# Optimization experiments

Measured on AMD Instinct MI355X. Metric: run time of the kernel, lower is better.

The kernel has to match this reference:

```python
import jax, jax.numpy as jnp
import numpy as np


def setup_inputs() -> dict:
    key = jax.random.key(0)
    k1, k2 = jax.random.split(key)
    B, C, M, N = 8, 3, 4096, 4096
    pc_src = jax.random.normal(k1, (B, C, M), dtype=jnp.float32)
    pc_dst = jax.random.normal(k2, (B, C, N), dtype=jnp.float32)
    return {"pc_src": pc_src, "pc_dst": pc_dst}


def reference(pc_src, pc_dst):
    # pc_src: [B,3,M], pc_dst: [B,3,N]
    # Pairwise Euclidean distance via ||s||^2 + ||d||^2 - 2 s.d (avoids Bx3xMxN tensor)
    s2 = jnp.sum(pc_src * pc_src, axis=1)              # [B,M]
    d2 = jnp.sum(pc_dst * pc_dst, axis=1)              # [B,N]
    cross = jnp.einsum('bcm,bcn->bmn', pc_src, pc_dst)  # [B,M,N]
    sq = s2[:, :, None] + d2[:, None, :] - 2.0 * cross
    diff = jnp.sqrt(jnp.maximum(sq, 0.0))              # [B,M,N] L2 distances
    forward_loss = jnp.mean(jnp.min(diff, axis=2))     # src -> dst nearest
    backward_loss = jnp.mean(jnp.min(diff, axis=1))    # dst -> src nearest
    chamfer_pure = forward_loss + backward_loss
    chamfer_weighted = chamfer_pure
    return (forward_loss + backward_loss, chamfer_pure, chamfer_weighted)
```

## Files before the change

kernel.cpp:

```cpp
#include <hip/hip_runtime.h>
#include <math.h>


constexpr int B = 8;
constexpr int M = 4096;

typedef __attribute__((ext_vector_type(8)))  short bf16x8;
typedef __attribute__((ext_vector_type(16))) float f32x16;

__device__ inline unsigned short bf16_of(float x) {
    unsigned int u = __float_as_uint(x);
    u += 0x7FFFu + ((u >> 16) & 1u);
    return (unsigned short)(u >> 16);
}
__device__ inline float bf16_to_f(unsigned short h) {
    return __uint_as_float(((unsigned int)h) << 16);
}


__global__ __launch_bounds__(256, 4) void chamfer_main(
    const float* __restrict__ src,
    const float* __restrict__ dst,
    float* __restrict__ part)
{
    int bid = blockIdx.x;
    const int cs  = bid & 1;  bid >>= 1;
    const int rg  = bid & 31; bid >>= 5;
    const int b   = bid & 7;  bid >>= 3;
    const int dir = bid;

    const float* __restrict__ qry = dir ? dst : src;
    const float* __restrict__ ref = dir ? src : dst;

    const int tid  = threadIdx.x;
    const int wave = tid >> 6;
    const int l31  = tid & 31;
    const int hf   = (tid >> 5) & 1;

    __shared__ __align__(16) unsigned short bstage[2][1024][8];
    __shared__ float bsum[8];

    bf16x8 afrag;
    {
        const int mrow = rg * 128 + wave * 32 + l31;
        const float* qb = qry + (size_t)b * 3 * M;
        const float x = qb[0 * M + mrow];
        const float y = qb[1 * M + mrow];
        const float z = qb[2 * M + mrow];
        const float s2 = x * x + y * y + z * z;
        const float xhf = bf16_to_f(bf16_of(x));
        const float yhf = bf16_to_f(bf16_of(y));
        const float zhf = bf16_to_f(bf16_of(z));
        const unsigned short nxh = bf16_of(-2.0f * xhf), nxl = bf16_of(-2.0f * (x - xhf));
        const unsigned short nyh = bf16_of(-2.0f * yhf), nyl = bf16_of(-2.0f * (y - yhf));
        const unsigned short nzh = bf16_of(-2.0f * zhf), nzl = bf16_of(-2.0f * (z - zhf));
        const unsigned short s2h = bf16_of(s2);
        const unsigned short s2l = bf16_of(s2 - bf16_to_f(s2h));
        const unsigned short one = 0x3F80;
        bf16x8 alo, ahi;
        alo[0]=(short)nxh; alo[1]=(short)nxh; alo[2]=(short)nxl; alo[3]=(short)nxl;
        alo[4]=(short)nyh; alo[5]=(short)nyh; alo[6]=(short)nyl; alo[7]=(short)nyl;
        ahi[0]=(short)nzh; ahi[1]=(short)nzh; ahi[2]=(short)nzl; ahi[3]=(short)nzl;
        ahi[4]=(short)s2h; ahi[5]=(short)s2l; ahi[6]=(short)one; ahi[7]=(short)one;
        afrag = hf ? ahi : alo;
    }

    f32x16 fwdE, fwdO;
#pragma unroll
    for (int r = 0; r < 16; ++r) { fwdE[r] = 3.0e38f; fwdO[r] = 3.0e38f; }

    const f32x16 zero = {};
    const float* rb = ref + (size_t)b * 3 * M + cs * 2048;

    for (int ch = 0; ch < 2; ++ch) {
        __syncthreads();
        {
            const int c0 = tid * 4;
            const float4 vx = *reinterpret_cast<const float4*>(&rb[0 * M + ch * 1024 + c0]);
            const float4 vy = *reinterpret_cast<const float4*>(&rb[1 * M + ch * 1024 + c0]);
            const float4 vz = *reinterpret_cast<const float4*>(&rb[2 * M + ch * 1024 + c0]);
            const float xs[4] = {vx.x, vx.y, vx.z, vx.w};
            const float ys[4] = {vy.x, vy.y, vy.z, vy.w};
            const float zs[4] = {vz.x, vz.y, vz.z, vz.w};
#pragma unroll
            for (int k = 0; k < 4; ++k) {
                const float x = xs[k], y = ys[k], z = zs[k];
                const float d2 = x * x + y * y + z * z;
                const unsigned short xh = bf16_of(x), xl = bf16_of(x - bf16_to_f(xh));
                const unsigned short yh = bf16_of(y), yl = bf16_of(y - bf16_to_f(yh));
                const unsigned short zh = bf16_of(z), zl = bf16_of(z - bf16_to_f(zh));
                const unsigned short d2h = bf16_of(d2);
                const unsigned short d2l = bf16_of(d2 - bf16_to_f(d2h));
                const unsigned short one = 0x3F80;
                bf16x8 v0, v1;
                v0[0]=(short)xh; v0[1]=(short)xl; v0[2]=(short)xh; v0[3]=(short)xl;
                v0[4]=(short)yh; v0[5]=(short)yl; v0[6]=(short)yh; v0[7]=(short)yl;
                v1[0]=(short)zh; v1[1]=(short)zl; v1[2]=(short)zh; v1[3]=(short)zl;
                v1[4]=(short)one; v1[5]=(short)one; v1[6]=(short)d2h; v1[7]=(short)d2l;
                *reinterpret_cast<bf16x8*>(&bstage[0][c0 + k][0]) = v0;
                *reinterpret_cast<bf16x8*>(&bstage[1][c0 + k][0]) = v1;
            }
        }
        __syncthreads();

#pragma unroll 4
        for (int i = 0; i < 16; ++i) {
            const bf16x8 bf0 = *reinterpret_cast<const bf16x8*>(&bstage[hf][i * 64 + l31][0]);
            const bf16x8 bf1 = *reinterpret_cast<const bf16x8*>(&bstage[hf][i * 64 + 32 + l31][0]);
            const f32x16 acc0 = __builtin_amdgcn_mfma_f32_32x32x16_bf16(afrag, bf0, zero, 0, 0, 0);
            const f32x16 acc1 = __builtin_amdgcn_mfma_f32_32x32x16_bf16(afrag, bf1, zero, 0, 0, 0);
#pragma unroll
            for (int r = 0; r < 16; ++r) {
                fwdE[r] = fminf(fwdE[r], acc0[r]);
                fwdO[r] = fminf(fwdO[r], acc1[r]);
            }
        }
    }

    f32x16 fwd;
#pragma unroll
    for (int r = 0; r < 16; ++r) fwd[r] = fminf(fwdE[r], fwdO[r]);

#pragma unroll
    for (int r = 0; r < 16; ++r) {
        float vv = fwd[r];
        vv = fminf(vv, __shfl_xor(vv, 1));
        vv = fminf(vv, __shfl_xor(vv, 2));
        vv = fminf(vv, __shfl_xor(vv, 4));
        vv = fminf(vv, __shfl_xor(vv, 8));
        vv = fminf(vv, __shfl_xor(vv, 16));
        fwd[r] = vv;
    }
    if (l31 == 0) {
        float* pf = part + ((size_t)cs * 16 + dir * 8 + b) * M
                  + rg * 128 + wave * 32 + hf * 4;
#pragma unroll
        for (int r = 0; r < 16; ++r)
            pf[(r & 3) + 8 * (r >> 2)] = fwd[r];
    }
    (void)bsum;
}

__global__ __launch_bounds__(256) void chamfer_reduce(
    const float* __restrict__ part, float* __restrict__ bsums)
{
    const int idx = blockIdx.x * 256 + threadIdx.x;
    const int row = idx & (M - 1);
    const int db  = idx >> 12;

    const float* p = part + (size_t)db * M + row;
    const float v = fminf(p[0], p[(size_t)16 * M]);

    float s = sqrtf(fmaxf(v, 0.0f));
#pragma unroll
    for (int off = 32; off > 0; off >>= 1) s += __shfl_down(s, off);
    __shared__ float partial[4];
    if ((threadIdx.x & 63) == 0) partial[threadIdx.x >> 6] = s;
    __syncthreads();
    if (threadIdx.x == 0)
        bsums[blockIdx.x] = partial[0] + partial[1] + partial[2] + partial[3];
}

__global__ __launch_bounds__(256) void chamfer_final(
    const float* __restrict__ bsums, float* __restrict__ out)
{
    float s = bsums[threadIdx.x];
#pragma unroll
    for (int off = 32; off > 0; off >>= 1) s += __shfl_down(s, off);
    __shared__ float partial[4];
    if ((threadIdx.x & 63) == 0) partial[threadIdx.x >> 6] = s;
    __syncthreads();
    if (threadIdx.x == 0) {
        const float tot = (partial[0] + partial[1] + partial[2] + partial[3])
                        * (1.0f / (float)(B * M));
        out[0] = tot;
        out[1] = tot;
        out[2] = tot;
    }
}

extern "C" void kernel_launch(void* const* d_in, const int* in_sizes, int n_in,
                              void* d_out, int out_size, void* d_ws, size_t ws_size,
                              hipStream_t stream)
{
    const float* src = (const float*)d_in[0];
    const float* dst = (const float*)d_in[1];
    float* out = (float*)d_out;

    float* part  = (float*)d_ws;
    float* bsums = (float*)((char*)d_ws + (1u << 19));

    chamfer_main  <<<1024, 256, 0, stream>>>(src, dst, part);
    chamfer_reduce<<<256, 256, 0, stream>>>(part, bsums);
    chamfer_final <<<1, 256, 0, stream>>>(bsums, out);
}
```

Measured before the change: 23.01 us.

## Split reference points four ways, swizzle LDS staging, and merge min accumulators

Each block now covers a quarter of the reference points instead of half, which doubles the grid to 2048 blocks and halves the LDS staging buffer. The reduce kernel takes the min over four partials instead of two. LDS rows are XOR-swizzled to cut bank conflicts on the MFMA operand reads, and the two min accumulators are folded into one to free registers for higher occupancy. In exchange it adds more partial traffic, more per-block query setup, and a larger workspace.

```diff
diff --git a/kernel.cpp b/kernel.cpp
--- a/kernel.cpp
+++ b/kernel.cpp
@@ -18,13 +18,13 @@
 }
 
 
-__global__ __launch_bounds__(256, 4) void chamfer_main(
+__global__ __launch_bounds__(256, 6) void chamfer_main(
     const float* __restrict__ src,
     const float* __restrict__ dst,
     float* __restrict__ part)
 {
     int bid = blockIdx.x;
-    const int cs  = bid & 1;  bid >>= 1;
+    const int cs  = bid & 3;  bid >>= 2;
     const int rg  = bid & 31; bid >>= 5;
     const int b   = bid & 7;  bid >>= 3;
     const int dir = bid;
@@ -37,8 +37,10 @@
     const int l31  = tid & 31;
     const int hf   = (tid >> 5) & 1;
 
-    __shared__ __align__(16) unsigned short bstage[2][1024][8];
-    __shared__ float bsum[8];
+    __shared__ __align__(16) unsigned short bstage[2][512][8];
+
+    const int sA = l31 ^ (l31 >> 3);
+    const int sB = 32 + (l31 ^ (4 + (l31 >> 3)));
 
     bf16x8 afrag;
     {
@@ -65,25 +67,25 @@
         afrag = hf ? ahi : alo;
     }
 
-    f32x16 fwdE, fwdO;
+    f32x16 fwd;
 #pragma unroll
-    for (int r = 0; r < 16; ++r) { fwdE[r] = 3.0e38f; fwdO[r] = 3.0e38f; }
+    for (int r = 0; r < 16; ++r) fwd[r] = 3.0e38f;
 
     const f32x16 zero = {};
-    const float* rb = ref + (size_t)b * 3 * M + cs * 2048;
+    const float* rb = ref + (size_t)b * 3 * M + cs * 1024;
 
     for (int ch = 0; ch < 2; ++ch) {
         __syncthreads();
         {
-            const int c0 = tid * 4;
-            const float4 vx = *reinterpret_cast<const float4*>(&rb[0 * M + ch * 1024 + c0]);
-            const float4 vy = *reinterpret_cast<const float4*>(&rb[1 * M + ch * 1024 + c0]);
-            const float4 vz = *reinterpret_cast<const float4*>(&rb[2 * M + ch * 1024 + c0]);
-            const float xs[4] = {vx.x, vx.y, vx.z, vx.w};
-            const float ys[4] = {vy.x, vy.y, vy.z, vy.w};
-            const float zs[4] = {vz.x, vz.y, vz.z, vz.w};
+            const int c0 = tid * 2;
+            const float2 vx = *reinterpret_cast<const float2*>(&rb[0 * M + ch * 512 + c0]);
+            const float2 vy = *reinterpret_cast<const float2*>(&rb[1 * M + ch * 512 + c0]);
+            const float2 vz = *reinterpret_cast<const float2*>(&rb[2 * M + ch * 512 + c0]);
+            const float xs[2] = {vx.x, vx.y};
+            const float ys[2] = {vy.x, vy.y};
+            const float zs[2] = {vz.x, vz.y};
 #pragma unroll
-            for (int k = 0; k < 4; ++k) {
+            for (int k = 0; k < 2; ++k) {
                 const float x = xs[k], y = ys[k], z = zs[k];
                 const float d2 = x * x + y * y + z * z;
                 const unsigned short xh = bf16_of(x), xl = bf16_of(x - bf16_to_f(xh));
@@ -97,29 +99,25 @@
                 v0[4]=(short)yh; v0[5]=(short)yl; v0[6]=(short)yh; v0[7]=(short)yl;
                 v1[0]=(short)zh; v1[1]=(short)zl; v1[2]=(short)zh; v1[3]=(short)zl;
                 v1[4]=(short)one; v1[5]=(short)one; v1[6]=(short)d2h; v1[7]=(short)d2l;
-                *reinterpret_cast<bf16x8*>(&bstage[0][c0 + k][0]) = v0;
-                *reinterpret_cast<bf16x8*>(&bstage[1][c0 + k][0]) = v1;
+                const int c = c0 + k;
+                const int swz = c ^ ((c >> 3) & 7);
+                *reinterpret_cast<bf16x8*>(&bstage[0][swz][0]) = v0;
+                *reinterpret_cast<bf16x8*>(&bstage[1][swz][0]) = v1;
             }
         }
         __syncthreads();
 
-#pragma unroll 4
-        for (int i = 0; i < 16; ++i) {
-            const bf16x8 bf0 = *reinterpret_cast<const bf16x8*>(&bstage[hf][i * 64 + l31][0]);
-            const bf16x8 bf1 = *reinterpret_cast<const bf16x8*>(&bstage[hf][i * 64 + 32 + l31][0]);
+#pragma unroll
+        for (int i = 0; i < 8; ++i) {
+            const bf16x8 bf0 = *reinterpret_cast<const bf16x8*>(&bstage[hf][i * 64 + sA][0]);
+            const bf16x8 bf1 = *reinterpret_cast<const bf16x8*>(&bstage[hf][i * 64 + sB][0]);
             const f32x16 acc0 = __builtin_amdgcn_mfma_f32_32x32x16_bf16(afrag, bf0, zero, 0, 0, 0);
             const f32x16 acc1 = __builtin_amdgcn_mfma_f32_32x32x16_bf16(afrag, bf1, zero, 0, 0, 0);
 #pragma unroll
-            for (int r = 0; r < 16; ++r) {
-                fwdE[r] = fminf(fwdE[r], acc0[r]);
-                fwdO[r] = fminf(fwdO[r], acc1[r]);
-            }
+            for (int r = 0; r < 16; ++r)
+                fwd[r] = fminf(fwd[r], fminf(acc0[r], acc1[r]));
         }
     }
-
-    f32x16 fwd;
-#pragma unroll
-    for (int r = 0; r < 16; ++r) fwd[r] = fminf(fwdE[r], fwdO[r]);
 
 #pragma unroll
     for (int r = 0; r < 16; ++r) {
@@ -138,7 +136,6 @@
         for (int r = 0; r < 16; ++r)
             pf[(r & 3) + 8 * (r >> 2)] = fwd[r];
     }
-    (void)bsum;
 }
 
 __global__ __launch_bounds__(256) void chamfer_reduce(
@@ -149,7 +146,8 @@
     const int db  = idx >> 12;
 
     const float* p = part + (size_t)db * M + row;
-    const float v = fminf(p[0], p[(size_t)16 * M]);
+    const float v = fminf(fminf(p[0],                  p[(size_t)16 * M]),
+                          fminf(p[(size_t)32 * M],     p[(size_t)48 * M]));
 
     float s = sqrtf(fmaxf(v, 0.0f));
 #pragma unroll
@@ -188,9 +186,9 @@
     float* out = (float*)d_out;
 
     float* part  = (float*)d_ws;
-    float* bsums = (float*)((char*)d_ws + (1u << 19));
+    float* bsums = (float*)((char*)d_ws + (1u << 20));
 
-    chamfer_main  <<<1024, 256, 0, stream>>>(src, dst, part);
+    chamfer_main  <<<2048, 256, 0, stream>>>(src, dst, part);
     chamfer_reduce<<<256, 256, 0, stream>>>(part, bsums);
     chamfer_final <<<1, 256, 0, stream>>>(bsums, out);
 }
```

New measurement: 31.93 us. 1.39x slower.

## Swizzle LDS staging and defer cross-lane min reduction to reduce kernel

Applied to the files above, without the earlier changes.

Reference-point fragments are now written to LDS with a swizzled row index, and the MFMA B-fragment reads use the matching addressing, to avoid bank conflicts. The main kernel no longer runs the five-step shuffle min across 32 lanes. Each lane writes its partial minima to a workspace 32 times larger, and the reduce kernel now reads 32 partials per row with float4 loads and takes their min. This trades the shuffle work in the main kernel for much more global memory write and read traffic (about 16 MB of partials), and the bsums offset moves to match.

```diff
diff --git a/kernel.cpp b/kernel.cpp
--- a/kernel.cpp
+++ b/kernel.cpp
@@ -38,7 +38,8 @@
     const int hf   = (tid >> 5) & 1;
 
     __shared__ __align__(16) unsigned short bstage[2][1024][8];
-    __shared__ float bsum[8];
+
+    const int lds_base = ((l31 & 7) << 7) + (l31 >> 3);
 
     bf16x8 afrag;
     {
@@ -97,16 +98,18 @@
                 v0[4]=(short)yh; v0[5]=(short)yl; v0[6]=(short)yh; v0[7]=(short)yl;
                 v1[0]=(short)zh; v1[1]=(short)zl; v1[2]=(short)zh; v1[3]=(short)zl;
                 v1[4]=(short)one; v1[5]=(short)one; v1[6]=(short)d2h; v1[7]=(short)d2l;
-                *reinterpret_cast<bf16x8*>(&bstage[0][c0 + k][0]) = v0;
-                *reinterpret_cast<bf16x8*>(&bstage[1][c0 + k][0]) = v1;
+                const int c = c0 + k;
+                const int swz = ((c & 7) << 7) + (c >> 3);
+                *reinterpret_cast<bf16x8*>(&bstage[0][swz][0]) = v0;
+                *reinterpret_cast<bf16x8*>(&bstage[1][swz][0]) = v1;
             }
         }
         __syncthreads();
 
 #pragma unroll 4
         for (int i = 0; i < 16; ++i) {
-            const bf16x8 bf0 = *reinterpret_cast<const bf16x8*>(&bstage[hf][i * 64 + l31][0]);
-            const bf16x8 bf1 = *reinterpret_cast<const bf16x8*>(&bstage[hf][i * 64 + 32 + l31][0]);
+            const bf16x8 bf0 = *reinterpret_cast<const bf16x8*>(&bstage[hf][lds_base + i * 8][0]);
+            const bf16x8 bf1 = *reinterpret_cast<const bf16x8*>(&bstage[hf][lds_base + i * 8 + 4][0]);
             const f32x16 acc0 = __builtin_amdgcn_mfma_f32_32x32x16_bf16(afrag, bf0, zero, 0, 0, 0);
             const f32x16 acc1 = __builtin_amdgcn_mfma_f32_32x32x16_bf16(afrag, bf1, zero, 0, 0, 0);
 #pragma unroll
@@ -117,28 +120,15 @@
         }
     }
 
-    f32x16 fwd;
-#pragma unroll
-    for (int r = 0; r < 16; ++r) fwd[r] = fminf(fwdE[r], fwdO[r]);
-
-#pragma unroll
-    for (int r = 0; r < 16; ++r) {
-        float vv = fwd[r];
-        vv = fminf(vv, __shfl_xor(vv, 1));
-        vv = fminf(vv, __shfl_xor(vv, 2));
-        vv = fminf(vv, __shfl_xor(vv, 4));
-        vv = fminf(vv, __shfl_xor(vv, 8));
-        vv = fminf(vv, __shfl_xor(vv, 16));
-        fwd[r] = vv;
-    }
-    if (l31 == 0) {
-        float* pf = part + ((size_t)cs * 16 + dir * 8 + b) * M
-                  + rg * 128 + wave * 32 + hf * 4;
-#pragma unroll
-        for (int r = 0; r < 16; ++r)
-            pf[(r & 3) + 8 * (r >> 2)] = fwd[r];
-    }
-    (void)bsum;
+    {
+        float* pf = part + (((size_t)cs * 16 + (size_t)dir * 8 + b) * 4096
+                            + rg * 128 + wave * 32 + hf * 4) * 32 + l31;
+#pragma unroll
+        for (int r = 0; r < 16; ++r) {
+            const float v = fminf(fwdE[r], fwdO[r]);
+            pf[(size_t)((r & 3) + 8 * (r >> 2)) * 32] = v;
+        }
+    }
 }
 
 __global__ __launch_bounds__(256) void chamfer_reduce(
@@ -148,8 +138,22 @@
     const int row = idx & (M - 1);
     const int db  = idx >> 12;
 
-    const float* p = part + (size_t)db * M + row;
-    const float v = fminf(p[0], p[(size_t)16 * M]);
+    const float4* p0 = reinterpret_cast<const float4*>(
+        part + ((size_t)(0 * 16 + db) * 4096 + row) * 32);
+    const float4* p1 = reinterpret_cast<const float4*>(
+        part + ((size_t)(1 * 16 + db) * 4096 + row) * 32);
+
+    float m0 = 3.0e38f, m1 = 3.0e38f, m2 = 3.0e38f, m3 = 3.0e38f;
+#pragma unroll
+    for (int j = 0; j < 8; ++j) {
+        const float4 a = p0[j];
+        const float4 b = p1[j];
+        m0 = fminf(m0, fminf(a.x, b.x));
+        m1 = fminf(m1, fminf(a.y, b.y));
+        m2 = fminf(m2, fminf(a.z, b.z));
+        m3 = fminf(m3, fminf(a.w, b.w));
+    }
+    const float v = fminf(fminf(m0, m1), fminf(m2, m3));
 
     float s = sqrtf(fmaxf(v, 0.0f));
 #pragma unroll
@@ -188,7 +192,7 @@
     float* out = (float*)d_out;
 
     float* part  = (float*)d_ws;
-    float* bsums = (float*)((char*)d_ws + (1u << 19));
+    float* bsums = (float*)((char*)d_ws + (16u << 20));
 
     chamfer_main  <<<1024, 256, 0, stream>>>(src, dst, part);
     chamfer_reduce<<<256, 256, 0, stream>>>(part, bsums);
```

Result: slower. 29.72 us (+29.1%).
